# Performance work log

Measured on AMD Instinct MI355X. Metric: run time of the kernel, lower is better.

## Reference

```python
import jax, jax.numpy as jnp
import numpy as np

BS, Q, NCLS, T = 16, 900, 1000, 100  # batch, queries, classes, targets per image
W_CLASS, W_BBOX, W_GIOU = 1.0, 1.0, 1.0


def _lsa_min(cost):
    """Jonker-Volgenant shortest-augmenting-path assignment (minimization).
    cost: [n, m] with n <= m. Returns (rows=arange(n), cols) matching
    scipy.optimize.linear_sum_assignment."""
    cost = np.asarray(cost, dtype=np.float64)
    n, m = cost.shape
    INF = np.inf
    u = np.zeros(n + 1)
    v = np.zeros(m + 1)
    p = np.zeros(m + 1, dtype=np.int64)   # p[j] = row (1-indexed) assigned to col j
    way = np.zeros(m + 1, dtype=np.int64)
    for i in range(1, n + 1):
        p[0] = i
        j0 = 0
        minv = np.full(m + 1, INF)
        used = np.zeros(m + 1, dtype=bool)
        while True:
            used[j0] = True
            i0 = p[j0]
            cur = cost[i0 - 1] - u[i0] - v[1:]
            free = ~used[1:]
            upd = free & (cur < minv[1:])
            minv[1:] = np.where(upd, cur, minv[1:])
            way[1:] = np.where(upd, j0, way[1:])
            free_idx = np.nonzero(free)[0]
            j1 = free_idx[np.argmin(minv[1:][free_idx])] + 1
            delta = minv[j1]
            used_idx = np.nonzero(used)[0]
            u[p[used_idx]] += delta
            v[used_idx] -= delta
            minv[1:][free] -= delta
            j0 = j1
            if p[j0] == 0:
                break
        while j0 != 0:
            j1 = way[j0]
            p[j0] = p[j1]
            j0 = j1
    cols = np.empty(n, dtype=np.int64)
    for j in range(1, m + 1):
        if p[j] > 0:
            cols[p[j] - 1] = j - 1
    return np.arange(n, dtype=np.int64), cols


def setup_inputs() -> dict:
    key = jax.random.key(0)
    k1, k2, k3, k4 = jax.random.split(key, 4)
    return {
        "pred_logits": jax.random.normal(k1, (BS, Q, NCLS), dtype=jnp.float32),
        "pred_boxes": jax.random.uniform(k2, (BS, Q, 4), dtype=jnp.float32),
        "tgt_ids": jax.random.randint(k3, (BS * T,), 0, NCLS, dtype=jnp.int64),
        "tgt_bbox": jax.random.uniform(k4, (BS * T, 4), dtype=jnp.float32),
    }


def _cost_matrix(pred_logits, pred_boxes, tgt_ids, tgt_bbox):
    out_prob = jax.nn.softmax(pred_logits.reshape(BS * Q, NCLS), axis=-1)
    out_bbox = pred_boxes.reshape(BS * Q, 4)
    cost_class = -out_prob[:, tgt_ids]                                   # [BS*Q, BS*T]
    cost_bbox = jnp.sum(jnp.abs(out_bbox[:, None, :] - tgt_bbox[None, :, :]), axis=-1)  # L1 cdist
    # cost_giou is zeros_like(cost_bbox) in the source, so its term vanishes
    Cm = W_BBOX * cost_bbox + W_CLASS * cost_class
    return Cm.reshape(BS, Q, BS * T)


def reference(pred_logits, pred_boxes, tgt_ids, tgt_bbox):
    Cm = _cost_matrix(pred_logits, pred_boxes, tgt_ids, tgt_bbox)
    Cnp = np.asarray(jax.device_get(Cm))
    idx_i, idx_j = [], []
    for b in range(BS):
        block = Cnp[b, :, b * T:(b + 1) * T]          # [Q, T], Q > T
        r, c = _lsa_min(block.T)                      # solve transpose: rows=targets, cols=preds
        order = np.argsort(c)                         # scipy sorts by prediction index
        idx_i.append(c[order])                        # selected prediction indices
        idx_j.append(r[order])                        # corresponding target indices
    return Cm, jnp.asarray(np.stack(idx_i)), jnp.asarray(np.stack(idx_j))
```

## Files before the change

### kernel.cpp

```cpp
#include <hip/hip_runtime.h>
#include <hip/hip_bf16.h>
#include <math.h>

#define BS   16
#define NQ   900
#define NCLS 1000
#define NT   100
#define MQ   900
#define NCOL (BS * NT)
#define NSLOT 15

typedef float f32x4 __attribute__((ext_vector_type(4)));

#define WAVE_FENCE() asm volatile("" ::: "memory")

__device__ __forceinline__ unsigned umin32(unsigned a, unsigned b) {
  return a < b ? a : b;
}

template <int CTRL>
__device__ __forceinline__ unsigned dpp_min_u32(unsigned x) {
  const unsigned o = (unsigned)__builtin_amdgcn_update_dpp(
      (int)x, (int)x, CTRL, 0xF, 0xF, false);
  return o < x ? o : x;
}

__device__ __forceinline__ unsigned wave_min_u32(unsigned x) {
  x = dpp_min_u32<0xB1>(x);
  x = dpp_min_u32<0x4E>(x);
  x = dpp_min_u32<0x114>(x);
  x = dpp_min_u32<0x118>(x);
  x = dpp_min_u32<0x142>(x);
  x = dpp_min_u32<0x143>(x);
  return (unsigned)__builtin_amdgcn_readlane((int)x, 63);
}

__device__ __forceinline__ unsigned f32key(float f) {
  unsigned e = __float_as_uint(f);
  return (e & 0x80000000u) ? ~e : (e | 0x80000000u);
}
__device__ __forceinline__ float f32unkey(unsigned k) {
  return __uint_as_float((k & 0x80000000u) ? (k ^ 0x80000000u) : ~k);
}

__device__ __forceinline__ int4 load_ids4(const int* __restrict__ ids, int c0,
                                          int id_stride) {
  if (id_stride == 1) {
    return *reinterpret_cast<const int4*>(ids + c0);
  } else {
    const int4 a = *reinterpret_cast<const int4*>(ids + 2 * c0);
    const int4 b = *reinterpret_cast<const int4*>(ids + 2 * c0 + 4);
    return make_int4(a.x, a.z, b.x, b.z);
  }
}

__global__ __launch_bounds__(256) void statcost_kernel(
    const float* __restrict__ logits, const float* __restrict__ boxes,
    const int* __restrict__ ids, const float* __restrict__ tbox,
    float* __restrict__ stats, float* __restrict__ costT, int id_stride) {
  const int tid = threadIdx.x, w = tid >> 6, lane = tid & 63;
  const int row = blockIdx.x * 4 + w;
  const int b = row / NQ;
  const int q = row - b * NQ;

  __shared__ float lbuf[4][NCLS];
  float* lr = lbuf[w];

  const float4* l4 = (const float4*)(logits + (size_t)row * NCLS);
  float4 vv[4];
  float lmax = -INFINITY;
#pragma unroll
  for (int it = 0; it < 4; ++it) {
    const int idx = it * 64 + lane;
    if (idx < NCLS / 4) {
      vv[it] = l4[idx];
      ((float4*)lr)[idx] = vv[it];
      lmax = fmaxf(lmax,
                   fmaxf(fmaxf(vv[it].x, vv[it].y), fmaxf(vv[it].z, vv[it].w)));
    }
  }
  for (int o = 32; o > 0; o >>= 1) lmax = fmaxf(lmax, __shfl_xor(lmax, o, 64));
  float psum = 0.f;
#pragma unroll
  for (int it = 0; it < 4; ++it) {
    const int idx = it * 64 + lane;
    if (idx < NCLS / 4) {
      psum += __expf(vv[it].x - lmax) + __expf(vv[it].y - lmax) +
              __expf(vv[it].z - lmax) + __expf(vv[it].w - lmax);
    }
  }
  for (int o = 32; o > 0; o >>= 1) psum += __shfl_xor(psum, o, 64);
  if (lane == 0) { stats[2 * row] = lmax; stats[2 * row + 1] = psum; }

  const float4 bb = *reinterpret_cast<const float4*>(boxes + (size_t)row * 4);
  const float inv = 1.f / psum;
  for (int rr = lane; rr < NT; rr += 64) {
    const int j = b * NT + rr;
    const int id = ids[(size_t)j * id_stride];
    const float4 tb = *reinterpret_cast<const float4*>(tbox + (size_t)j * 4);
    float d = fabsf(bb.x - tb.x);
    d += fabsf(bb.y - tb.y);
    d += fabsf(bb.z - tb.z);
    d += fabsf(bb.w - tb.w);
    costT[((size_t)b * NT + rr) * MQ + q] = d - __expf(lr[id] - lmax) * inv;
  }
}

__global__ __launch_bounds__(64) void rowmin_kernel(
    const float* __restrict__ costT, float* __restrict__ u_w,
    int* __restrict__ amin_w) {
  const int bid = blockIdx.x;
  const float* rowp = costT + (size_t)bid * MQ;
  const int lane = threadIdx.x;
  const unsigned UMAX = 0xFFFFFFFFu;

  unsigned tv[NSLOT];
#pragma unroll
  for (int s = 0; s < NSLOT; ++s) {
    const int c = s * 64 + lane;
    tv[s] = (c < MQ) ? f32key(rowp[c]) : UMAX;
  }
  unsigned m[NSLOT];
#pragma unroll
  for (int s = 0; s < NSLOT; ++s) m[s] = tv[s];
#pragma unroll
  for (int st = 1; st < NSLOT; st <<= 1) {
#pragma unroll
    for (int s = 0; s + st < NSLOT; s += 2 * st) m[s] = umin32(m[s], m[s + st]);
  }
  const unsigned s_vb = wave_min_u32(m[0]);
  unsigned cj[NSLOT];
#pragma unroll
  for (int s = 0; s < NSLOT; ++s)
    cj[s] = (tv[s] == s_vb) ? (unsigned)(s * 64 + lane) : UMAX;
#pragma unroll
  for (int st = 1; st < NSLOT; st <<= 1) {
#pragma unroll
    for (int s = 0; s + st < NSLOT; s += 2 * st)
      cj[s] = umin32(cj[s], cj[s + st]);
  }
  const unsigned s_j = wave_min_u32(cj[0]);
  if (lane == 0) { u_w[bid] = f32unkey(s_vb); amin_w[bid] = (int)s_j; }
}

__global__ __launch_bounds__(256) void main_kernel(
    const float* __restrict__ logits, const float* __restrict__ boxes,
    const int* __restrict__ ids, const float* __restrict__ tbox,
    const float* __restrict__ stats, const float* __restrict__ costT,
    const float* __restrict__ u_w, const int* __restrict__ amin_w,
    float* __restrict__ C, float* __restrict__ out_i,
    float* __restrict__ out_j, int id_stride) {
  __shared__ float lbuf[4][NCLS];
  __shared__ int p[MQ + 1];
  __shared__ int way[MQ + 65];
  __shared__ int cols[NT];

  if (blockIdx.x >= BS) {
    const int tid = threadIdx.x, w = tid >> 6, lane = tid & 63;
    const int row = (blockIdx.x - BS) * 4 + w;
    float* lr = lbuf[w];
    const float4* l4 = (const float4*)(logits + (size_t)row * NCLS);
#pragma unroll
    for (int it = 0; it < 4; ++it) {
      const int idx = it * 64 + lane;
      if (idx < NCLS / 4) ((float4*)lr)[idx] = l4[idx];
    }
    const float rmax = stats[2 * row];
    const float inv = 1.f / stats[2 * row + 1];
    const float4 bb = *reinterpret_cast<const float4*>(boxes + (size_t)row * 4);
    float* crow = C + (size_t)row * NCOL;
#pragma unroll
    for (int it = 0; it < 6; ++it) {
      const int c0 = it * 256 + lane * 4;
      const int4 id4 = load_ids4(ids, c0, id_stride);
      const float4 tb0 = *reinterpret_cast<const float4*>(tbox + (size_t)c0 * 4);
      const float4 tb1 =
          *reinterpret_cast<const float4*>(tbox + (size_t)(c0 + 1) * 4);
      const float4 tb2 =
          *reinterpret_cast<const float4*>(tbox + (size_t)(c0 + 2) * 4);
      const float4 tb3 =
          *reinterpret_cast<const float4*>(tbox + (size_t)(c0 + 3) * 4);
      f32x4 outv;
      {
        float d = fabsf(bb.x - tb0.x) + fabsf(bb.y - tb0.y) +
                  fabsf(bb.z - tb0.z) + fabsf(bb.w - tb0.w);
        outv.x = d - __expf(lr[id4.x] - rmax) * inv;
      }
      {
        float d = fabsf(bb.x - tb1.x) + fabsf(bb.y - tb1.y) +
                  fabsf(bb.z - tb1.z) + fabsf(bb.w - tb1.w);
        outv.y = d - __expf(lr[id4.y] - rmax) * inv;
      }
      {
        float d = fabsf(bb.x - tb2.x) + fabsf(bb.y - tb2.y) +
                  fabsf(bb.z - tb2.z) + fabsf(bb.w - tb2.w);
        outv.z = d - __expf(lr[id4.z] - rmax) * inv;
      }
      {
        float d = fabsf(bb.x - tb3.x) + fabsf(bb.y - tb3.y) +
                  fabsf(bb.z - tb3.z) + fabsf(bb.w - tb3.w);
        outv.w = d - __expf(lr[id4.w] - rmax) * inv;
      }
      __builtin_nontemporal_store(outv,
                                  reinterpret_cast<f32x4*>(crow + c0));
    }
    {
      const int c = 1536 + lane;
      const int id = ids[(size_t)c * id_stride];
      const float4 tb = *reinterpret_cast<const float4*>(tbox + (size_t)c * 4);
      float d = fabsf(bb.x - tb.x) + fabsf(bb.y - tb.y) + fabsf(bb.z - tb.z) +
                fabsf(bb.w - tb.w);
      __builtin_nontemporal_store(d - __expf(lr[id] - rmax) * inv, crow + c);
    }
    return;
  }

  if (threadIdx.x >= 64) return;
  const int b = blockIdx.x;
  const float* cost = costT + (size_t)b * NT * MQ;
  const int lane = threadIdx.x;
  const float FINF = __builtin_inff();
  const unsigned UMAX = 0xFFFFFFFFu;
  const unsigned UINFB = 0x7F800000u;

  float v[NSLOT];
  unsigned V32[NSLOT];
  float cfA[NSLOT], cfB[NSLOT];
  int jp[NSLOT];

#pragma unroll
  for (int s = 0; s < NSLOT; ++s) v[s] = 0.f;
  for (int j = lane; j <= MQ; j += 64) p[j] = 0;
  for (int r2 = lane; r2 < NT; r2 += 64) cols[r2] = -7777;
  WAVE_FENCE();

  float u0 = u_w[b * NT + lane];
  float u1 = (lane < NT - 64) ? u_w[b * NT + 64 + lane] : 0.f;
  const int a0 = amin_w[b * NT + lane];
  const int a1 = (lane < NT - 64) ? amin_w[b * NT + 64 + lane] : 0;

  unsigned long long cl0 = 0, cl1 = 0;
  {
    unsigned clm = 0;
    for (int r2 = 0; r2 < NT; ++r2) {
      const int aj0 = (r2 < 64) ? __builtin_amdgcn_readlane(a0, r2)
                                : __builtin_amdgcn_readlane(a1, r2 - 64);
      const int slot = aj0 >> 6;
      const bool owner = (lane == (aj0 & 63));
      const unsigned long long bl = __ballot(owner && ((clm >> slot) & 1u));
      if (bl == 0) {
        if (owner) { clm |= 1u << slot; p[aj0 + 1] = r2 + 1; }
        if (r2 < 64) cl0 |= 1ull << r2;
        else         cl1 |= 1ull << (r2 - 64);
      }
    }
  }
  WAVE_FENCE();

#pragma unroll
  for (int s = 0; s < NSLOT; ++s) {
    const int c = s * 64 + lane;
    if (c < MQ) jp[s] = ((c + 1) << 7) | p[c + 1];
  }

  for (int i = 1; i <= NT; ++i) {
    const int r = i - 1;
    const bool skip = (r < 64) ? ((cl0 >> r) & 1ull) : ((cl1 >> (r - 64)) & 1ull);
    if (skip) continue;

    {
      const float* crow = cost + (size_t)r * MQ;
#pragma unroll
      for (int s = 0; s < NSLOT; ++s) {
        const int c = s * 64 + lane;
        cfA[s] = (c < MQ) ? crow[c] : FINF;
      }
    }
    float uir;
    {
      const float uu = (r < 64) ? u0 : u1;
      uir = __uint_as_float(
          (unsigned)__builtin_amdgcn_readlane((int)__float_as_uint(uu),
                                              r & 63));
    }

    unsigned usedm = (lane >= MQ - 14 * 64) ? (1u << 14) : 0u;
    int tm0 = 0, tm1 = 0;
    float D = 0.f;
#pragma unroll
    for (int s = 0; s < NSLOT; ++s) V32[s] = UINFB;
    if (lane == 0) p[0] = i;
    WAVE_FENCE();

    int j0 = 0;
    int i0 = i;
    float ui0 = uir;

    auto iterate = [&](float (&CUR)[NSLOT], float (&NXT)[NSLOT]) -> bool {
      if (j0 > 0) {
        const int cz = j0 - 1;
        const bool own = (lane == (cz & 63));
        usedm |= own ? (1u << (cz >> 6)) : 0u;
      }
      {
        const int ri = i0 - 1;
        tm0 |= (lane == ri) ? 1 : 0;
        tm1 |= (lane == (ri - 64)) ? 1 : 0;
      }

      const float a = ui0 - D;
      unsigned tv[NSLOT];
#pragma unroll
      for (int s = 0; s < NSLOT; ++s) {
        const bool us = (usedm >> s) & 1u;
        const float rel = fmaxf(CUR[s] - a - v[s], 0.f);
        const unsigned rb = __float_as_uint(rel);
        const unsigned rbg = us ? UMAX : rb;
        const bool upd = rbg < V32[s];
        way[upd ? (s * 64 + lane + 1) : 0] = j0;
        V32[s] = upd ? rbg : V32[s];
        tv[s] = us ? UMAX : V32[s];
      }
      unsigned m[NSLOT];
#pragma unroll
      for (int s = 0; s < NSLOT; ++s) m[s] = tv[s];
#pragma unroll
      for (int st = 1; st < NSLOT; st <<= 1) {
#pragma unroll
        for (int s = 0; s + st < NSLOT; s += 2 * st)
          m[s] = umin32(m[s], m[s + st]);
      }
      const unsigned s_best = wave_min_u32(m[0]);
      const float Dnew = __uint_as_float(s_best);

      unsigned cj[NSLOT];
#pragma unroll
      for (int s = 0; s < NSLOT; ++s)
        cj[s] = (tv[s] == s_best) ? (unsigned)jp[s] : UMAX;
#pragma unroll
      for (int st = 1; st < NSLOT; st <<= 1) {
#pragma unroll
        for (int s = 0; s + st < NSLOT; s += 2 * st)
          cj[s] = umin32(cj[s], cj[s + st]);
      }
      const unsigned jpw = wave_min_u32(cj[0]);
      const int j1 = (int)(jpw >> 7);
      const int pj1 = (int)(jpw & 127u);

      if (pj1 != 0) {
        const float* crow = cost + (size_t)(pj1 - 1) * MQ;
#pragma unroll
        for (int s = 0; s < NSLOT; ++s) {
          const int c = s * 64 + lane;
          NXT[s] = (c < MQ) ? crow[c] : FINF;
        }
      }
      float unext = 0.f;
      if (pj1 != 0) {
        const int rr2 = pj1 - 1;
        const float uu = (rr2 < 64) ? u0 : u1;
        unext = __uint_as_float(
            (unsigned)__builtin_amdgcn_readlane((int)__float_as_uint(uu),
                                                rr2 & 63));
      }

      const float delta = Dnew - D;
      D = Dnew;
      u0 += tm0 ? delta : 0.f;
      u1 += tm1 ? delta : 0.f;

      j0 = j1; i0 = pj1; ui0 = unext;
      return pj1 != 0;
    };

    while (true) {
      if (!iterate(cfA, cfB)) break;
      if (!iterate(cfB, cfA)) break;
    }

    {
      const float Dend = D;
#pragma unroll
      for (int s = 0; s < NSLOT; ++s) {
        const int c = s * 64 + lane;
        const bool us = (usedm >> s) & 1u;
        const float dv = __uint_as_float(V32[s]) - Dend;
        v[s] += (us && c < MQ) ? dv : 0.f;
      }
    }

    WAVE_FENCE();
    if (lane == 0) {
      int ja = j0;
      while (ja != 0) { const int jb = way[ja]; p[ja] = p[jb]; ja = jb; }
    }
    WAVE_FENCE();
#pragma unroll
    for (int s = 0; s < NSLOT; ++s) {
      const int c = s * 64 + lane;
      if (c < MQ) jp[s] = ((c + 1) << 7) | p[c + 1];
    }
  }

  WAVE_FENCE();
  for (int j = lane + 1; j <= MQ; j += 64)
    if (p[j] > 0) cols[p[j] - 1] = j - 1;
  WAVE_FENCE();

  for (int r = lane; r < NT; r += 64) {
    const int c = cols[r];
    int rank = 0;
    for (int r2 = 0; r2 < NT; ++r2) rank += (cols[r2] < c);
    out_i[b * NT + rank] = (float)c;
    out_j[b * NT + rank] = (float)r;
  }
}

extern "C" void kernel_launch(void* const* d_in, const int* in_sizes, int n_in,
                              void* d_out, int out_size, void* d_ws,
                              size_t ws_size, hipStream_t stream) {
  const float* logits = (const float*)d_in[0];
  const float* boxes  = (const float*)d_in[1];
  const int*   ids    = (const int*)d_in[2];
  const float* tbox   = (const float*)d_in[3];

  float* C     = (float*)d_out;
  float* out_i = C + (size_t)BS * NQ * NCOL;
  float* out_j = out_i + NCOL;

  float* costT = (float*)d_ws;
  float* stats = costT + (size_t)BS * NT * MQ;
  float* u_w   = stats + 2 * BS * NQ;
  int*   amin_w = (int*)(u_w + BS * NT);

  const int id_stride = (in_sizes[2] == 2 * NCOL) ? 2 : 1;

  statcost_kernel<<<BS * NQ / 4, 256, 0, stream>>>(logits, boxes, ids, tbox,
                                                   stats, costT, id_stride);
  rowmin_kernel<<<BS * NT, 64, 0, stream>>>(costT, u_w, amin_w);
  main_kernel<<<BS * NQ / 4 + BS, 256, 0, stream>>>(
      logits, boxes, ids, tbox, stats, costT, u_w, amin_w, C, out_i, out_j,
      id_stride);
}
```

Baseline: 83.63 us.

## Split fused LSA/cost-write kernel into separate LSA and C-write kernels

Replaces the combined main kernel, which ran the per-image assignment solver in 16 blocks alongside the cost-matrix write blocks, with two kernels launched back to back: a 64-thread LSA kernel and a dedicated C-write kernel. The C-write kernel also stages target ids into shared memory once per block instead of loading them per element. The aim is to give each kernel its own launch bounds and resource usage. The cost is that the C-matrix write no longer overlaps the serial LSA and is instead serialized after it on the stream.

```diff
diff --git a/kernel.cpp b/kernel.cpp
--- a/kernel.cpp
+++ b/kernel.cpp
@@ -41,17 +41,6 @@
 }
 __device__ __forceinline__ float f32unkey(unsigned k) {
   return __uint_as_float((k & 0x80000000u) ? (k ^ 0x80000000u) : ~k);
-}
-
-__device__ __forceinline__ int4 load_ids4(const int* __restrict__ ids, int c0,
-                                          int id_stride) {
-  if (id_stride == 1) {
-    return *reinterpret_cast<const int4*>(ids + c0);
-  } else {
-    const int4 a = *reinterpret_cast<const int4*>(ids + 2 * c0);
-    const int4 b = *reinterpret_cast<const int4*>(ids + 2 * c0 + 4);
-    return make_int4(a.x, a.z, b.x, b.z);
-  }
 }
 
 __global__ __launch_bounds__(256) void statcost_kernel(
@@ -143,79 +132,14 @@
   if (lane == 0) { u_w[bid] = f32unkey(s_vb); amin_w[bid] = (int)s_j; }
 }
 
-__global__ __launch_bounds__(256) void main_kernel(
-    const float* __restrict__ logits, const float* __restrict__ boxes,
-    const int* __restrict__ ids, const float* __restrict__ tbox,
-    const float* __restrict__ stats, const float* __restrict__ costT,
-    const float* __restrict__ u_w, const int* __restrict__ amin_w,
-    float* __restrict__ C, float* __restrict__ out_i,
-    float* __restrict__ out_j, int id_stride) {
-  __shared__ float lbuf[4][NCLS];
+__global__ __launch_bounds__(64) void lsa_kernel(
+    const float* __restrict__ costT, const float* __restrict__ u_w,
+    const int* __restrict__ amin_w, float* __restrict__ out_i,
+    float* __restrict__ out_j) {
   __shared__ int p[MQ + 1];
   __shared__ int way[MQ + 65];
   __shared__ int cols[NT];
 
-  if (blockIdx.x >= BS) {
-    const int tid = threadIdx.x, w = tid >> 6, lane = tid & 63;
-    const int row = (blockIdx.x - BS) * 4 + w;
-    float* lr = lbuf[w];
-    const float4* l4 = (const float4*)(logits + (size_t)row * NCLS);
-#pragma unroll
-    for (int it = 0; it < 4; ++it) {
-      const int idx = it * 64 + lane;
-      if (idx < NCLS / 4) ((float4*)lr)[idx] = l4[idx];
-    }
-    const float rmax = stats[2 * row];
-    const float inv = 1.f / stats[2 * row + 1];
-    const float4 bb = *reinterpret_cast<const float4*>(boxes + (size_t)row * 4);
-    float* crow = C + (size_t)row * NCOL;
-#pragma unroll
-    for (int it = 0; it < 6; ++it) {
-      const int c0 = it * 256 + lane * 4;
-      const int4 id4 = load_ids4(ids, c0, id_stride);
-      const float4 tb0 = *reinterpret_cast<const float4*>(tbox + (size_t)c0 * 4);
-      const float4 tb1 =
-          *reinterpret_cast<const float4*>(tbox + (size_t)(c0 + 1) * 4);
-      const float4 tb2 =
-          *reinterpret_cast<const float4*>(tbox + (size_t)(c0 + 2) * 4);
-      const float4 tb3 =
-          *reinterpret_cast<const float4*>(tbox + (size_t)(c0 + 3) * 4);
-      f32x4 outv;
-      {
-        float d = fabsf(bb.x - tb0.x) + fabsf(bb.y - tb0.y) +
-                  fabsf(bb.z - tb0.z) + fabsf(bb.w - tb0.w);
-        outv.x = d - __expf(lr[id4.x] - rmax) * inv;
-      }
-      {
-        float d = fabsf(bb.x - tb1.x) + fabsf(bb.y - tb1.y) +
-                  fabsf(bb.z - tb1.z) + fabsf(bb.w - tb1.w);
-        outv.y = d - __expf(lr[id4.y] - rmax) * inv;
-      }
-      {
-        float d = fabsf(bb.x - tb2.x) + fabsf(bb.y - tb2.y) +
-                  fabsf(bb.z - tb2.z) + fabsf(bb.w - tb2.w);
-        outv.z = d - __expf(lr[id4.z] - rmax) * inv;
-      }
-      {
-        float d = fabsf(bb.x - tb3.x) + fabsf(bb.y - tb3.y) +
-                  fabsf(bb.z - tb3.z) + fabsf(bb.w - tb3.w);
-        outv.w = d - __expf(lr[id4.w] - rmax) * inv;
-      }
-      __builtin_nontemporal_store(outv,
-                                  reinterpret_cast<f32x4*>(crow + c0));
-    }
-    {
-      const int c = 1536 + lane;
-      const int id = ids[(size_t)c * id_stride];
-      const float4 tb = *reinterpret_cast<const float4*>(tbox + (size_t)c * 4);
-      float d = fabsf(bb.x - tb.x) + fabsf(bb.y - tb.y) + fabsf(bb.z - tb.z) +
-                fabsf(bb.w - tb.w);
-      __builtin_nontemporal_store(d - __expf(lr[id] - rmax) * inv, crow + c);
-    }
-    return;
-  }
-
-  if (threadIdx.x >= 64) return;
   const int b = blockIdx.x;
   const float* cost = costT + (size_t)b * NT * MQ;
   const int lane = threadIdx.x;
@@ -416,6 +340,74 @@
   }
 }
 
+__global__ __launch_bounds__(256) void cwrite_kernel(
+    const float* __restrict__ logits, const float* __restrict__ boxes,
+    const int* __restrict__ ids, const float* __restrict__ tbox,
+    const float* __restrict__ stats, float* __restrict__ C, int id_stride) {
+  const int tid = threadIdx.x, w = tid >> 6, lane = tid & 63;
+  const int row = blockIdx.x * 4 + w;
+  __shared__ float lbuf[4][NCLS];
+  __shared__ int ids_s[NCOL];
+
+  for (int c = tid; c < NCOL; c += 256) ids_s[c] = ids[(size_t)c * id_stride];
+
+  float* lr = lbuf[w];
+  const float4* l4 = (const float4*)(logits + (size_t)row * NCLS);
+#pragma unroll
+  for (int it = 0; it < 4; ++it) {
+    const int idx = it * 64 + lane;
+    if (idx < NCLS / 4) ((float4*)lr)[idx] = l4[idx];
+  }
+  __syncthreads();
+
+  const float rmax = stats[2 * row];
+  const float inv = 1.f / stats[2 * row + 1];
+  const float4 bb = *reinterpret_cast<const float4*>(boxes + (size_t)row * 4);
+  float* crow = C + (size_t)row * NCOL;
+#pragma unroll
+  for (int it = 0; it < 6; ++it) {
+    const int c0 = it * 256 + lane * 4;
+    const int4 id4 = *reinterpret_cast<const int4*>(&ids_s[c0]);
+    const float4 tb0 = *reinterpret_cast<const float4*>(tbox + (size_t)c0 * 4);
+    const float4 tb1 =
+        *reinterpret_cast<const float4*>(tbox + (size_t)(c0 + 1) * 4);
+    const float4 tb2 =
+        *reinterpret_cast<const float4*>(tbox + (size_t)(c0 + 2) * 4);
+    const float4 tb3 =
+        *reinterpret_cast<const float4*>(tbox + (size_t)(c0 + 3) * 4);
+    f32x4 outv;
+    {
+      float d = fabsf(bb.x - tb0.x) + fabsf(bb.y - tb0.y) +
+                fabsf(bb.z - tb0.z) + fabsf(bb.w - tb0.w);
+      outv.x = d - __expf(lr[id4.x] - rmax) * inv;
+    }
+    {
+      float d = fabsf(bb.x - tb1.x) + fabsf(bb.y - tb1.y) +
+                fabsf(bb.z - tb1.z) + fabsf(bb.w - tb1.w);
+      outv.y = d - __expf(lr[id4.y] - rmax) * inv;
+    }
+    {
+      float d = fabsf(bb.x - tb2.x) + fabsf(bb.y - tb2.y) +
+                fabsf(bb.z - tb2.z) + fabsf(bb.w - tb2.w);
+      outv.z = d - __expf(lr[id4.z] - rmax) * inv;
+    }
+    {
+      float d = fabsf(bb.x - tb3.x) + fabsf(bb.y - tb3.y) +
+                fabsf(bb.z - tb3.z) + fabsf(bb.w - tb3.w);
+      outv.w = d - __expf(lr[id4.w] - rmax) * inv;
+    }
+    __builtin_nontemporal_store(outv, reinterpret_cast<f32x4*>(crow + c0));
+  }
+  {
+    const int c = 1536 + lane;
+    const int id = ids_s[c];
+    const float4 tb = *reinterpret_cast<const float4*>(tbox + (size_t)c * 4);
+    float d = fabsf(bb.x - tb.x) + fabsf(bb.y - tb.y) + fabsf(bb.z - tb.z) +
+              fabsf(bb.w - tb.w);
+    __builtin_nontemporal_store(d - __expf(lr[id] - rmax) * inv, crow + c);
+  }
+}
+
 extern "C" void kernel_launch(void* const* d_in, const int* in_sizes, int n_in,
                               void* d_out, int out_size, void* d_ws,
                               size_t ws_size, hipStream_t stream) {
@@ -438,7 +430,7 @@
   statcost_kernel<<<BS * NQ / 4, 256, 0, stream>>>(logits, boxes, ids, tbox,
                                                    stats, costT, id_stride);
   rowmin_kernel<<<BS * NT, 64, 0, stream>>>(costT, u_w, amin_w);
-  main_kernel<<<BS * NQ / 4 + BS, 256, 0, stream>>>(
-      logits, boxes, ids, tbox, stats, costT, u_w, amin_w, C, out_i, out_j,
-      id_stride);
-}
+  lsa_kernel<<<BS, 64, 0, stream>>>(costT, u_w, amin_w, out_i, out_j);
+  cwrite_kernel<<<BS * NQ / 4, 256, 0, stream>>>(logits, boxes, ids, tbox,
+                                                 stats, C, id_stride);
+}
```

After: 121.7 us. 1.46x slower.

## Add auction-style augmenting row reduction before shortest-path augmentation

Applied to the files above, without the earlier changes.

Inserts a Jonker-Volgenant augmenting row reduction phase after the column-reduction/greedy step. For each still-free row it finds the two smallest reduced costs with wave reductions, assigns the row to the best column, lowers that column's price and re-queues any displaced row, with a cap of 256 steps. Only rows left unassigned then go through the expensive shortest-augmenting-path loop. This aims to cut the serial augmentation work, at the cost of extra per-step reductions, and it relies on the dual updates staying consistent with the later phase.

```diff
diff --git a/kernel.cpp b/kernel.cpp
--- a/kernel.cpp
+++ b/kernel.cpp
@@ -41,17 +41,6 @@
 }
 __device__ __forceinline__ float f32unkey(unsigned k) {
   return __uint_as_float((k & 0x80000000u) ? (k ^ 0x80000000u) : ~k);
-}
-
-__device__ __forceinline__ int4 load_ids4(const int* __restrict__ ids, int c0,
-                                          int id_stride) {
-  if (id_stride == 1) {
-    return *reinterpret_cast<const int4*>(ids + c0);
-  } else {
-    const int4 a = *reinterpret_cast<const int4*>(ids + 2 * c0);
-    const int4 b = *reinterpret_cast<const int4*>(ids + 2 * c0 + 4);
-    return make_int4(a.x, a.z, b.x, b.z);
-  }
 }
 
 __global__ __launch_bounds__(256) void statcost_kernel(
@@ -172,7 +161,14 @@
 #pragma unroll
     for (int it = 0; it < 6; ++it) {
       const int c0 = it * 256 + lane * 4;
-      const int4 id4 = load_ids4(ids, c0, id_stride);
+      int4 id4;
+      if (id_stride == 1) {
+        id4 = *reinterpret_cast<const int4*>(ids + c0);
+      } else {
+        const int4 a = *reinterpret_cast<const int4*>(ids + 2 * c0);
+        const int4 bq = *reinterpret_cast<const int4*>(ids + 2 * c0 + 4);
+        id4 = make_int4(a.x, a.z, bq.x, bq.z);
+      }
       const float4 tb0 = *reinterpret_cast<const float4*>(tbox + (size_t)c0 * 4);
       const float4 tb1 =
           *reinterpret_cast<const float4*>(tbox + (size_t)(c0 + 1) * 4);
@@ -201,8 +197,7 @@
                   fabsf(bb.z - tb3.z) + fabsf(bb.w - tb3.w);
         outv.w = d - __expf(lr[id4.w] - rmax) * inv;
       }
-      __builtin_nontemporal_store(outv,
-                                  reinterpret_cast<f32x4*>(crow + c0));
+      __builtin_nontemporal_store(outv, reinterpret_cast<f32x4*>(crow + c0));
     }
     {
       const int c = 1536 + lane;
@@ -257,6 +252,101 @@
   }
   WAVE_FENCE();
 
+  unsigned long long f0 = ~cl0;
+  unsigned long long f1 = (~cl1) & ((1ull << (NT - 64)) - 1);
+  {
+    int steps = 0;
+    while ((f0 | f1) && steps < 256) {
+      ++steps;
+      int r;
+      if (f0) { r = __builtin_ctzll(f0); f0 &= f0 - 1; }
+      else    { r = 64 + __builtin_ctzll(f1); f1 &= f1 - 1; }
+
+      const float* crow = cost + (size_t)r * MQ;
+      unsigned k1[NSLOT];
+#pragma unroll
+      for (int s = 0; s < NSLOT; ++s) {
+        const int c = s * 64 + lane;
+        const float cf = (c < MQ) ? crow[c] : FINF;
+        k1[s] = (c < MQ) ? f32key(cf - v[s]) : UMAX;
+      }
+      unsigned m[NSLOT];
+#pragma unroll
+      for (int s = 0; s < NSLOT; ++s) m[s] = k1[s];
+#pragma unroll
+      for (int st = 1; st < NSLOT; st <<= 1) {
+#pragma unroll
+        for (int s = 0; s + st < NSLOT; s += 2 * st)
+          m[s] = umin32(m[s], m[s + st]);
+      }
+      const unsigned mk1 = wave_min_u32(m[0]);
+      unsigned cj[NSLOT];
+#pragma unroll
+      for (int s = 0; s < NSLOT; ++s)
+        cj[s] = (k1[s] == mk1) ? (unsigned)(s * 64 + lane) : UMAX;
+#pragma unroll
+      for (int st = 1; st < NSLOT; st <<= 1) {
+#pragma unroll
+        for (int s = 0; s + st < NSLOT; s += 2 * st)
+          cj[s] = umin32(cj[s], cj[s + st]);
+      }
+      const int j1 = (int)wave_min_u32(cj[0]);
+
+      unsigned q[NSLOT];
+#pragma unroll
+      for (int s = 0; s < NSLOT; ++s)
+        q[s] = ((s * 64 + lane) == j1) ? UMAX : k1[s];
+      unsigned qm[NSLOT];
+#pragma unroll
+      for (int s = 0; s < NSLOT; ++s) qm[s] = q[s];
+#pragma unroll
+      for (int st = 1; st < NSLOT; st <<= 1) {
+#pragma unroll
+        for (int s = 0; s + st < NSLOT; s += 2 * st)
+          qm[s] = umin32(qm[s], qm[s + st]);
+      }
+      const unsigned mk2 = wave_min_u32(qm[0]);
+      unsigned cq[NSLOT];
+#pragma unroll
+      for (int s = 0; s < NSLOT; ++s)
+        cq[s] = (q[s] == mk2) ? (unsigned)(s * 64 + lane) : UMAX;
+#pragma unroll
+      for (int st = 1; st < NSLOT; st <<= 1) {
+#pragma unroll
+        for (int s = 0; s + st < NSLOT; s += 2 * st)
+          cq[s] = umin32(cq[s], cq[s + st]);
+      }
+      const int j2 = (int)wave_min_u32(cq[0]);
+
+      const float u1f = f32unkey(mk1);
+      const float u2f = f32unkey(mk2);
+
+      WAVE_FENCE();
+      int jt = j1;
+      int own = p[jt + 1];
+      if (mk1 != mk2) {
+        const int s1 = jt >> 6, l1 = jt & 63;
+        const float dv = u2f - u1f;
+#pragma unroll
+        for (int s = 0; s < NSLOT; ++s)
+          v[s] -= (s == s1 && lane == l1) ? dv : 0.f;
+      } else if (own != 0) {
+        jt = j2;
+        own = p[jt + 1];
+      }
+      if (r < 64) u0 = (lane == r) ? u2f : u0;
+      else        u1 = (lane == (r - 64)) ? u2f : u1;
+
+      if (lane == 0) p[jt + 1] = r + 1;
+      WAVE_FENCE();
+      if (own != 0) {
+        const int k = own - 1;
+        if (k < 64) f0 |= 1ull << k;
+        else        f1 |= 1ull << (k - 64);
+      }
+    }
+  }
+
 #pragma unroll
   for (int s = 0; s < NSLOT; ++s) {
     const int c = s * 64 + lane;
@@ -265,8 +355,9 @@
 
   for (int i = 1; i <= NT; ++i) {
     const int r = i - 1;
-    const bool skip = (r < 64) ? ((cl0 >> r) & 1ull) : ((cl1 >> (r - 64)) & 1ull);
-    if (skip) continue;
+    const bool need =
+        (r < 64) ? ((f0 >> r) & 1ull) : ((f1 >> (r - 64)) & 1ull);
+    if (!need) continue;
 
     {
       const float* crow = cost + (size_t)r * MQ;
```

After: 88.79 us. +6.2%, slower.
